# Kernel optimization log

Measured on AMD Instinct MI355X. Metric: run time of the kernel, lower is better.

## Reference

```python
import jax, jax.numpy as jnp
import numpy as np
from jax import lax

BATCH = 4096
HID = 512
T = 20


def setup_inputs() -> dict:
    key = jax.random.key(0)
    ks = jax.random.split(key, 12)
    B2 = BATCH * 2
    inp = {
        "x": jax.random.normal(ks[0], (BATCH, 2, T, 2), jnp.float32),
        "x_agents": jax.random.normal(ks[1], (BATCH, 2), jnp.float32),  # unused by forward
        "h0": jax.random.normal(ks[2], (B2, HID), jnp.float32),
        "c0": jax.random.normal(ks[3], (B2, HID), jnp.float32),
        # LSTMCell params (PyTorch layout: gates stacked as [i, f, g, o])
        "W_ih": jax.random.normal(ks[4], (4 * HID, 2), jnp.float32) * 0.05,
        "W_hh": jax.random.normal(ks[5], (4 * HID, HID), jnp.float32) * 0.05,
        "b_ih": jax.random.normal(ks[6], (4 * HID,), jnp.float32) * 0.05,
        "b_hh": jax.random.normal(ks[7], (4 * HID,), jnp.float32) * 0.05,
        # MLP head
        "fc1_w": jax.random.normal(ks[8], (HID, 2 * T * HID), jnp.float32) * 0.01,
        "fc1_b": jax.random.normal(ks[9], (HID,), jnp.float32) * 0.01,
        "fc2_w": jax.random.normal(ks[10], (1, HID), jnp.float32) * 0.05,
        "fc2_b": jax.random.normal(ks[11], (1,), jnp.float32) * 0.05,
        "training_step": 2,
    }
    return inp


def reference(x, x_agents, h0, c0, W_ih, W_hh, b_ih, b_hh, fc1_w, fc1_b, fc2_w, fc2_b, training_step):
    # training_step == 2 path (default) of the original module.
    batch = x.shape[0]
    H = W_hh.shape[1]
    xs = x.reshape(batch * 2, T, 2).transpose(1, 0, 2)  # [T, B2, 2]

    def step(carry, xt):
        h, c = carry
        gates = xt @ W_ih.T + b_ih + h @ W_hh.T + b_hh  # [B2, 4H]
        i, f, g, o = jnp.split(gates, 4, axis=-1)
        i = jax.nn.sigmoid(i)
        f = jax.nn.sigmoid(f)
        g = jnp.tanh(g)
        o = jax.nn.sigmoid(o)
        c_new = f * c + i * g
        h_new = o * jnp.tanh(c_new)
        return (h_new, c_new), h_new

    _, hs = lax.scan(step, (h0, c0), xs)  # hs: [T, B2, H]
    states = hs.transpose(1, 0, 2).reshape(batch, 2 * T * H)  # [batch, 2*T*H]
    out = jax.nn.relu(states @ fc1_w.T + fc1_b) @ fc2_w.T + fc2_b
    return jax.nn.sigmoid(out)
```

## Files before the change

### kernel.cpp

```cpp
#include <hip/hip_runtime.h>
#include <hip/hip_bf16.h>

#define TSTEPS 20
#define SMEM_BYTES 131072

typedef __bf16 bf16x8 __attribute__((ext_vector_type(8)));
typedef float f32x4 __attribute__((ext_vector_type(4)));
typedef unsigned short u16;

__device__ __forceinline__ u16 f2bf(float f) {
  unsigned u = __builtin_bit_cast(unsigned, f);
  u = (u + 0x7FFFu + ((u >> 16) & 1u)) >> 16;
  return (u16)u;
}
__device__ __forceinline__ float rcp_(float v) { return __builtin_amdgcn_rcpf(v); }
__device__ __forceinline__ float sig_(float v) { return rcp_(1.f + __expf(-v)); }
__device__ __forceinline__ float tanh_(float v) { return 1.f - 2.f * rcp_(1.f + __expf(2.f * v)); }

#define MFMA16(a, b, c) __builtin_amdgcn_mfma_f32_16x16x32_bf16((a), (b), (c), 0, 0, 0)
#define BAR() asm volatile("s_barrier" ::: "memory")
#define WAITV(n) asm volatile("s_waitcnt vmcnt(" #n ")" ::: "memory")
#define WAITLG() asm volatile("s_waitcnt lgkmcnt(0)" ::: "memory")

__device__ __forceinline__ void gload16(const u16* g, u16* lds) {
#if defined(__HIP_DEVICE_COMPILE__)
  __builtin_amdgcn_global_load_lds(
      (const __attribute__((address_space(1))) unsigned*)g,
      (__attribute__((address_space(3))) unsigned*)lds, 16, 0, 0);
#endif
}

__global__ void convert_f32_bf16(const float* __restrict__ s, u16* __restrict__ d, int n) {
  int i = (blockIdx.x * blockDim.x + threadIdx.x) * 4;
  if (i + 3 < n) {
    float4 v = *reinterpret_cast<const float4*>(s + i);
    ushort4 o;
    o.x = f2bf(v.x); o.y = f2bf(v.y); o.z = f2bf(v.z); o.w = f2bf(v.w);
    *reinterpret_cast<ushort4*>(d + i) = o;
  }
}

__global__ void convert_whh_p(const float* __restrict__ w, u16* __restrict__ d) {
  int p = blockIdx.x;
  int k = threadIdx.x;
  int j = p & 15, f = (p >> 4) & 3, wg = (p >> 6) & 3, s = p >> 8;
  int orig = (f << 9) + (s << 6) + (wg << 4) + j;
  d[p * 512 + k] = f2bf(w[orig * 512 + k]);
}

__global__ void bx_prep(const float* __restrict__ Wih, const float* __restrict__ bih,
                        const float* __restrict__ bhh, u16* __restrict__ Bx) {
  int p = blockIdx.x * blockDim.x + threadIdx.x;
  if (p >= 2048) return;
  int j = p & 15, f = (p >> 4) & 3, wg = (p >> 6) & 3, s = p >> 8;
  int o = (f << 9) + (s << 6) + (wg << 4) + j;
  u16* row = Bx + p * 32;
  row[0] = f2bf(Wih[o * 2 + 0]);
  row[1] = f2bf(Wih[o * 2 + 1]);
  row[2] = f2bf(bih[o] + bhh[o]);
#pragma unroll
  for (int k = 3; k < 32; ++k) row[k] = 0;
}

__global__ void init_state(const float* __restrict__ h0, const float* __restrict__ c0,
                           u16* __restrict__ hbf, float* __restrict__ cws,
                           float* __restrict__ acc, int n, int nacc) {
  int i = blockIdx.x * blockDim.x + threadIdx.x;
  if (i < n) { hbf[i] = f2bf(h0[i]); cws[i] = c0[i]; }
  if (i < nacc) acc[i] = 0.f;
}

__global__ __launch_bounds__(512, 1) void step256(
    const u16* __restrict__ Wp,
    const u16* __restrict__ Bxg,
    const float* __restrict__ x,
    const u16* __restrict__ hin,
    u16* __restrict__ hout,
    float* __restrict__ c,
    const u16* __restrict__ fc1w,
    float* __restrict__ facc,
    int t, int doLstm, int doFc1) {
  extern __shared__ char S[];

  const int tid = threadIdx.x;
  const int lane = tid & 63, wid = tid >> 6;
  const int jl = lane & 15, kg = lane >> 4;
  const int bid = blockIdx.x;
  const int s = (bid >> 3) & 7;
  const int nb = (bid & 7) * 4 + (bid >> 6);
  const int n0 = nb * 256;
  const int srow = tid >> 3;
  const int sw = (tid & 7) ^ (srow & 7);

  if (doLstm) {
    const int wm = wid >> 2, wn = wid & 3;
    const int u = s * 64 + wn * 16 + jl;
    const int swz0 = (kg ^ (jl & 7)) * 16;
    const int swz1 = ((4 + kg) ^ (jl & 7)) * 16;
    const int aB0 = wm * 16384 + jl * 128 + swz0;
    const int aB1 = wm * 16384 + jl * 128 + swz1;
    const int bB0 = 32768 + wn * 8192 + jl * 128 + swz0;
    const int bB1 = 32768 + wn * 8192 + jl * 128 + swz1;
    const u16* srcA = hin + (n0 + srow) * 512 + sw * 8;
    const u16* srcB = Wp + (s * 256 + srow) * 512 + sw * 8;

    f32x4 acc[8][4];
#pragma unroll
    for (int mt = 0; mt < 8; ++mt)
#pragma unroll
      for (int f = 0; f < 4; ++f) acc[mt][f] = (f32x4){0.f, 0.f, 0.f, 0.f};

    float2 xv = {0.f, 0.f};
    if (tid < 256) xv = *reinterpret_cast<const float2*>(x + (n0 + tid) * 40 + t * 2);
    {
      const int r0 = tid >> 2, ch = tid & 3;
      gload16(Bxg + (s * 256 + 0 * 128 + r0) * 32 + ch * 8, (u16*)(S + 32768 + 0 * 8192 + wid * 1024));
      gload16(Bxg + (s * 256 + 1 * 128 + r0) * 32 + ch * 8, (u16*)(S + 32768 + 1 * 8192 + wid * 1024));
    }
#pragma unroll
    for (int q = 0; q < 4; ++q) {
      gload16(srcA + q * 32768, (u16*)(S + 65536 + q * 8192 + wid * 1024));
      gload16(srcB + q * 32768, (u16*)(S + 65536 + 32768 + q * 8192 + wid * 1024));
    }
    if (tid < 256) {
      u16 row0[8] = {f2bf(xv.x), f2bf(xv.y), 0x3F80u, 0, 0, 0, 0, 0};
      *reinterpret_cast<uint4*>(S + tid * 64) = *reinterpret_cast<const uint4*>(row0);
      uint4 z = {0u, 0u, 0u, 0u};
      *reinterpret_cast<uint4*>(S + tid * 64 + 16) = z;
      *reinterpret_cast<uint4*>(S + tid * 64 + 32) = z;
      *reinterpret_cast<uint4*>(S + tid * 64 + 48) = z;
    }
    WAITLG();
    WAITV(8);
    BAR();
    {
#pragma unroll
      for (int mt = 0; mt < 8; ++mt) {
        bf16x8 a = *reinterpret_cast<const bf16x8*>(S + (wm * 128 + mt * 16 + jl) * 64 + kg * 16);
#pragma unroll
        for (int f = 0; f < 4; ++f) {
          bf16x8 b = *reinterpret_cast<const bf16x8*>(S + 32768 + (wn * 64 + f * 16 + jl) * 64 + kg * 16);
          acc[mt][f] = MFMA16(a, b, acc[mt][f]);
        }
      }
    }
    BAR();

#define LSTAGE(kt, p)                                                              \
  do {                                                                             \
    _Pragma("unroll") for (int q = 0; q < 4; ++q) {                                \
      gload16(srcA + q * 32768 + (kt) * 64, (u16*)(S + (p) * 65536 + q * 8192 + wid * 1024)); \
      gload16(srcB + q * 32768 + (kt) * 64, (u16*)(S + (p) * 65536 + 32768 + q * 8192 + wid * 1024)); \
    }                                                                              \
  } while (0)
#define LCOMP(p)                                                                   \
  do {                                                                             \
    bf16x8 a0[8], b0[4];                                                           \
    _Pragma("unroll") for (int mt = 0; mt < 8; ++mt)                               \
        a0[mt] = *reinterpret_cast<const bf16x8*>(S + (p) * 65536 + aB0 + mt * 2048); \
    _Pragma("unroll") for (int f = 0; f < 4; ++f)                                  \
        b0[f] = *reinterpret_cast<const bf16x8*>(S + (p) * 65536 + bB0 + f * 2048); \
    _Pragma("unroll") for (int mt = 0; mt < 8; ++mt)                               \
      _Pragma("unroll") for (int f = 0; f < 4; ++f)                                \
        acc[mt][f] = MFMA16(a0[mt], b0[f], acc[mt][f]);                            \
    _Pragma("unroll") for (int mt = 0; mt < 8; ++mt)                               \
        a0[mt] = *reinterpret_cast<const bf16x8*>(S + (p) * 65536 + aB1 + mt * 2048); \
    _Pragma("unroll") for (int f = 0; f < 4; ++f)                                  \
        b0[f] = *reinterpret_cast<const bf16x8*>(S + (p) * 65536 + bB1 + f * 2048); \
    _Pragma("unroll") for (int mt = 0; mt < 8; ++mt)                               \
      _Pragma("unroll") for (int f = 0; f < 4; ++f)                                \
        acc[mt][f] = MFMA16(a0[mt], b0[f], acc[mt][f]);                            \
  } while (0)

#pragma unroll
    for (int kt = 0; kt < 8; ++kt) {
      if (kt < 7) {
        if ((kt + 1) & 1) LSTAGE(kt + 1, 0); else LSTAGE(kt + 1, 1);
        WAITV(8);
      } else {
        WAITV(0);
      }
      BAR();
      if (kt & 1) LCOMP(0); else LCOMP(1);
      BAR();
    }

    float cv[8][4];
#pragma unroll
    for (int mt = 0; mt < 8; ++mt)
#pragma unroll
      for (int r = 0; r < 4; ++r)
        cv[mt][r] = c[(n0 + wm * 128 + mt * 16 + kg * 4 + r) * 512 + u];
#pragma unroll
    for (int mt = 0; mt < 8; ++mt)
#pragma unroll
      for (int r = 0; r < 4; ++r) {
        int n = n0 + wm * 128 + mt * 16 + kg * 4 + r;
        float iv = sig_(acc[mt][0][r]);
        float fv = sig_(acc[mt][1][r]);
        float gv = tanh_(acc[mt][2][r]);
        float ov = sig_(acc[mt][3][r]);
        float cn = fv * cv[mt][r] + iv * gv;
        c[n * 512 + u] = cn;
        hout[n * 512 + u] = f2bf(ov * tanh_(cn));
      }
  }

  if (doFc1) {
    const int Fm0 = nb * 128, Fj0 = s * 64;
    const int Fwm = wid >> 1, Fwn = wid & 1;
    const int tf = t - 1;
    const int swz0 = (kg ^ (jl & 7)) * 16;
    const int swz1 = ((4 + kg) ^ (jl & 7)) * 16;
    const int faB0 = Fwm * 4096 + jl * 128 + swz0;
    const int faB1 = Fwm * 4096 + jl * 128 + swz1;
    const int fbB0 = 16384 + Fwn * 4096 + jl * 128 + swz0;
    const int fbB1 = 16384 + Fwn * 4096 + jl * 128 + swz1;
    const u16* fsrcA = hin + 2 * (Fm0 + srow) * 512 + sw * 8;
    const u16* fsrcB = fc1w + (Fj0 + srow) * 20480 + tf * 512 + sw * 8;

    f32x4 fa[2][2];
#pragma unroll
    for (int a = 0; a < 2; ++a)
#pragma unroll
      for (int b = 0; b < 2; ++b) fa[a][b] = (f32x4){0.f, 0.f, 0.f, 0.f};

#define FSTAGE(kt, p)                                                              \
  do {                                                                             \
    const int an_ = (kt) >> 3, kc_ = ((kt) & 7) * 64;                              \
    gload16(fsrcA + 0 * 65536 + an_ * 512 + kc_, (u16*)(S + (p) * 32768 + 0 * 8192 + wid * 1024)); \
    gload16(fsrcA + 1 * 65536 + an_ * 512 + kc_, (u16*)(S + (p) * 32768 + 1 * 8192 + wid * 1024)); \
    gload16(fsrcB + an_ * 10240 + kc_, (u16*)(S + (p) * 32768 + 16384 + wid * 1024)); \
  } while (0)
#define FCOMP(p)                                                                   \
  do {                                                                             \
    bf16x8 af[2], bf[2];                                                           \
    _Pragma("unroll") for (int mf = 0; mf < 2; ++mf)                               \
        af[mf] = *reinterpret_cast<const bf16x8*>(S + (p) * 32768 + faB0 + mf * 2048); \
    _Pragma("unroll") for (int jf = 0; jf < 2; ++jf)                               \
        bf[jf] = *reinterpret_cast<const bf16x8*>(S + (p) * 32768 + fbB0 + jf * 2048); \
    _Pragma("unroll") for (int mf = 0; mf < 2; ++mf)                               \
      _Pragma("unroll") for (int jf = 0; jf < 2; ++jf)                             \
        fa[mf][jf] = MFMA16(af[mf], bf[jf], fa[mf][jf]);                           \
    _Pragma("unroll") for (int mf = 0; mf < 2; ++mf)                               \
        af[mf] = *reinterpret_cast<const bf16x8*>(S + (p) * 32768 + faB1 + mf * 2048); \
    _Pragma("unroll") for (int jf = 0; jf < 2; ++jf)                               \
        bf[jf] = *reinterpret_cast<const bf16x8*>(S + (p) * 32768 + fbB1 + jf * 2048); \
    _Pragma("unroll") for (int mf = 0; mf < 2; ++mf)                               \
      _Pragma("unroll") for (int jf = 0; jf < 2; ++jf)                             \
        fa[mf][jf] = MFMA16(af[mf], bf[jf], fa[mf][jf]);                           \
  } while (0)

    FSTAGE(0, 0);
#pragma unroll
    for (int kt = 0; kt < 16; ++kt) {
      if (kt < 15) {
        if ((kt + 1) & 1) FSTAGE(kt + 1, 1); else FSTAGE(kt + 1, 0);
        WAITV(3);
      } else {
        WAITV(0);
      }
      BAR();
      if (kt & 1) FCOMP(1); else FCOMP(0);
      BAR();
    }
#pragma unroll
    for (int mf = 0; mf < 2; ++mf)
#pragma unroll
      for (int jf = 0; jf < 2; ++jf) {
        int j = Fj0 + Fwn * 32 + jf * 16 + jl;
#pragma unroll
        for (int r = 0; r < 4; ++r) {
          int m = Fm0 + Fwm * 32 + mf * 16 + kg * 4 + r;
          facc[m * 512 + j] += fa[mf][jf][r];
        }
      }
  }
}

__global__ __launch_bounds__(256) void head_kernel(
    const float* __restrict__ acc, const float* __restrict__ fc1b,
    const float* __restrict__ fc2w, const float* __restrict__ fc2b,
    float* __restrict__ out) {
  int lane = threadIdx.x & 63;
  int row = blockIdx.x * 4 + (threadIdx.x >> 6);
  float sum = 0.f;
#pragma unroll
  for (int j = lane; j < 512; j += 64)
    sum += fmaxf(acc[row * 512 + j] + fc1b[j], 0.f) * fc2w[j];
#pragma unroll
  for (int off = 32; off; off >>= 1) sum += __shfl_down(sum, off);
  if (lane == 0) out[row] = sig_(sum + fc2b[0]);
}

extern "C" void kernel_launch(void* const* d_in, const int* in_sizes, int n_in,
                              void* d_out, int out_size, void* d_ws, size_t ws_size,
                              hipStream_t stream) {
  const float* x = (const float*)d_in[0];
  const float* h0 = (const float*)d_in[2];
  const float* c0 = (const float*)d_in[3];
  const float* Wih = (const float*)d_in[4];
  const float* Whh = (const float*)d_in[5];
  const float* bih = (const float*)d_in[6];
  const float* bhh = (const float*)d_in[7];
  const float* fc1w = (const float*)d_in[8];
  const float* fc1b = (const float*)d_in[9];
  const float* fc2w = (const float*)d_in[10];
  const float* fc2b = (const float*)d_in[11];
  float* out = (float*)d_out;

  char* ws = (char*)d_ws;
  const size_t MB = 1 << 20;
  u16* Wp = (u16*)(ws);
  u16* fc1_bf = (u16*)(ws + 2 * MB);
  u16* hbf0 = (u16*)(ws + 22 * MB);
  u16* hbf1 = (u16*)(ws + 30 * MB);
  float* cws = (float*)(ws + 38 * MB);
  float* facc = (float*)(ws + 54 * MB);
  u16* Bxg = (u16*)(ws + 62 * MB);

  (void)hipFuncSetAttribute(reinterpret_cast<const void*>(step256),
                            hipFuncAttributeMaxDynamicSharedMemorySize, SMEM_BYTES);

  convert_whh_p<<<2048, 512, 0, stream>>>(Whh, Wp);
  bx_prep<<<8, 256, 0, stream>>>(Wih, bih, bhh, Bxg);
  convert_f32_bf16<<<10240, 256, 0, stream>>>(fc1w, fc1_bf, 512 * 20480);
  init_state<<<16384, 256, 0, stream>>>(h0, c0, hbf0, cws, facc, 8192 * 512, 4096 * 512);

  u16* hb[2] = {hbf0, hbf1};
  for (int t = 0; t <= TSTEPS; ++t) {
    step256<<<256, 512, SMEM_BYTES, stream>>>(
        Wp, Bxg, x, hb[t & 1], hb[(t + 1) & 1], cws, fc1_bf, facc,
        t, t < TSTEPS ? 1 : 0, t > 0 ? 1 : 0);
  }
  head_kernel<<<1024, 256, 0, stream>>>(facc, fc1b, fc2w, fc2b, out);
}
```

Baseline: 632.5 us.

## Pre-pack weights into MFMA fragment order and load B operands directly to registers

Weights W_hh and fc1 are repacked once into the exact per-lane MFMA fragment layout, so the step kernel reads B operands straight from global memory into registers instead of staging them through LDS. This halves LDS use (static 64KB instead of 128KB dynamic) and removes the B-side LDS traffic and async copies. The cell state is also stored in a lane-contiguous layout so each thread does vectorized float4 loads and stores of c. The trade-off is more global/L2 load latency on the critical MFMA path, since B fragments are fetched per iteration without LDS double buffering.

```diff
diff --git a/kernel.cpp b/kernel.cpp
--- a/kernel.cpp
+++ b/kernel.cpp
@@ -2,7 +2,6 @@
 #include <hip/hip_bf16.h>
 
 #define TSTEPS 20
-#define SMEM_BYTES 131072
 
 typedef __bf16 bf16x8 __attribute__((ext_vector_type(8)));
 typedef float f32x4 __attribute__((ext_vector_type(4)));
@@ -30,22 +29,37 @@
 #endif
 }
 
-__global__ void convert_f32_bf16(const float* __restrict__ s, u16* __restrict__ d, int n) {
-  int i = (blockIdx.x * blockDim.x + threadIdx.x) * 4;
-  if (i + 3 < n) {
-    float4 v = *reinterpret_cast<const float4*>(s + i);
-    ushort4 o;
-    o.x = f2bf(v.x); o.y = f2bf(v.y); o.z = f2bf(v.z); o.w = f2bf(v.w);
-    *reinterpret_cast<ushort4*>(d + i) = o;
-  }
-}
-
-__global__ void convert_whh_p(const float* __restrict__ w, u16* __restrict__ d) {
-  int p = blockIdx.x;
-  int k = threadIdx.x;
-  int j = p & 15, f = (p >> 4) & 3, wg = (p >> 6) & 3, s = p >> 8;
-  int orig = (f << 9) + (s << 6) + (wg << 4) + j;
-  d[p * 512 + k] = f2bf(w[orig * 512 + k]);
+__global__ void wp2_prep(const float* __restrict__ w, u16* __restrict__ d) {
+  int id = blockIdx.x * blockDim.x + threadIdx.x;
+  int jl = id & 15, t1 = id >> 4;
+  int kg = t1 & 3, t2 = t1 >> 2;
+  int f = t2 & 3, t3 = t2 >> 2;
+  int wn = t3 & 3, t4 = t3 >> 2;
+  int kkg = t4 & 15, s = t4 >> 4;
+  const float* src = w + (f * 512 + s * 64 + wn * 16 + jl) * 512 + kkg * 32 + kg * 8;
+  float4 v0 = *reinterpret_cast<const float4*>(src);
+  float4 v1 = *reinterpret_cast<const float4*>(src + 4);
+  u16* dst = d + id * 8;
+  dst[0] = f2bf(v0.x); dst[1] = f2bf(v0.y); dst[2] = f2bf(v0.z); dst[3] = f2bf(v0.w);
+  dst[4] = f2bf(v1.x); dst[5] = f2bf(v1.y); dst[6] = f2bf(v1.z); dst[7] = f2bf(v1.w);
+}
+
+__global__ void fc1p_prep(const float* __restrict__ w, u16* __restrict__ d) {
+  int id = blockIdx.x * blockDim.x + threadIdx.x;
+  int jl = id & 15, t1 = id >> 4;
+  int kg = t1 & 3, t2 = t1 >> 2;
+  int jf = t2 & 1, t3 = t2 >> 1;
+  int Fwn = t3 & 1, t4 = t3 >> 1;
+  int kk2 = t4 & 31, t5 = t4 >> 5;
+  int tf = t5 % 20, s = t5 / 20;
+  int j = s * 64 + Fwn * 32 + jf * 16 + jl;
+  int k = kk2 * 32 + kg * 8;
+  const float* src = w + j * 20480 + (k >> 9) * 10240 + tf * 512 + (k & 511);
+  float4 v0 = *reinterpret_cast<const float4*>(src);
+  float4 v1 = *reinterpret_cast<const float4*>(src + 4);
+  u16* dst = d + id * 8;
+  dst[0] = f2bf(v0.x); dst[1] = f2bf(v0.y); dst[2] = f2bf(v0.z); dst[3] = f2bf(v0.w);
+  dst[4] = f2bf(v1.x); dst[5] = f2bf(v1.y); dst[6] = f2bf(v1.z); dst[7] = f2bf(v1.w);
 }
 
 __global__ void bx_prep(const float* __restrict__ Wih, const float* __restrict__ bih,
@@ -64,23 +78,32 @@
 
 __global__ void init_state(const float* __restrict__ h0, const float* __restrict__ c0,
                            u16* __restrict__ hbf, float* __restrict__ cws,
-                           float* __restrict__ acc, int n, int nacc) {
+                           float* __restrict__ facc, int nh, int nacc) {
   int i = blockIdx.x * blockDim.x + threadIdx.x;
-  if (i < n) { hbf[i] = f2bf(h0[i]); cws[i] = c0[i]; }
-  if (i < nacc) acc[i] = 0.f;
+  if (i < nh) {
+    hbf[i] = f2bf(h0[i]);
+    int r = i & 3, mt = (i >> 2) & 7, lane = (i >> 5) & 63, wid = (i >> 11) & 7, bid = i >> 14;
+    int s = (bid >> 3) & 7, nb = (bid & 7) * 4 + (bid >> 6);
+    int wm = wid >> 2, wn = wid & 3;
+    int jl = lane & 15, kg = lane >> 4;
+    int n = nb * 256 + wm * 128 + mt * 16 + kg * 4 + r;
+    int u = s * 64 + wn * 16 + jl;
+    cws[i] = c0[n * 512 + u];
+  }
+  if (i < nacc) facc[i] = 0.f;
 }
 
 __global__ __launch_bounds__(512, 1) void step256(
-    const u16* __restrict__ Wp,
+    const u16* __restrict__ Wp2,
     const u16* __restrict__ Bxg,
     const float* __restrict__ x,
     const u16* __restrict__ hin,
     u16* __restrict__ hout,
-    float* __restrict__ c,
-    const u16* __restrict__ fc1w,
+    float* __restrict__ cws,
+    const u16* __restrict__ fc1p,
     float* __restrict__ facc,
     int t, int doLstm, int doFc1) {
-  extern __shared__ char S[];
+  __shared__ char S[65536];
 
   const int tid = threadIdx.x;
   const int lane = tid & 63, wid = tid >> 6;
@@ -91,18 +114,16 @@
   const int n0 = nb * 256;
   const int srow = tid >> 3;
   const int sw = (tid & 7) ^ (srow & 7);
+  const int swz0 = (kg ^ (jl & 7)) * 16;
+  const int swz1 = ((4 + kg) ^ (jl & 7)) * 16;
 
   if (doLstm) {
     const int wm = wid >> 2, wn = wid & 3;
     const int u = s * 64 + wn * 16 + jl;
-    const int swz0 = (kg ^ (jl & 7)) * 16;
-    const int swz1 = ((4 + kg) ^ (jl & 7)) * 16;
     const int aB0 = wm * 16384 + jl * 128 + swz0;
     const int aB1 = wm * 16384 + jl * 128 + swz1;
-    const int bB0 = 32768 + wn * 8192 + jl * 128 + swz0;
-    const int bB1 = 32768 + wn * 8192 + jl * 128 + swz1;
     const u16* srcA = hin + (n0 + srow) * 512 + sw * 8;
-    const u16* srcB = Wp + (s * 256 + srow) * 512 + sw * 8;
+    const u16* bl = Wp2 + s * 131072 + wn * 2048 + kg * 128 + jl * 8;
 
     f32x4 acc[8][4];
 #pragma unroll
@@ -112,112 +133,105 @@
 
     float2 xv = {0.f, 0.f};
     if (tid < 256) xv = *reinterpret_cast<const float2*>(x + (n0 + tid) * 40 + t * 2);
-    {
-      const int r0 = tid >> 2, ch = tid & 3;
-      gload16(Bxg + (s * 256 + 0 * 128 + r0) * 32 + ch * 8, (u16*)(S + 32768 + 0 * 8192 + wid * 1024));
-      gload16(Bxg + (s * 256 + 1 * 128 + r0) * 32 + ch * 8, (u16*)(S + 32768 + 1 * 8192 + wid * 1024));
-    }
-#pragma unroll
-    for (int q = 0; q < 4; ++q) {
-      gload16(srcA + q * 32768, (u16*)(S + 65536 + q * 8192 + wid * 1024));
-      gload16(srcB + q * 32768, (u16*)(S + 65536 + 32768 + q * 8192 + wid * 1024));
-    }
+    gload16(Bxg + (s * 256 + (tid >> 2)) * 32 + (tid & 3) * 8,
+            (u16*)(S + 49152 + wid * 1024));
+    gload16(Bxg + (s * 256 + 128 + (tid >> 2)) * 32 + (tid & 3) * 8,
+            (u16*)(S + 49152 + 8192 + wid * 1024));
+#pragma unroll
+    for (int q = 0; q < 4; ++q)
+      gload16(srcA + q * 32768, (u16*)(S + q * 8192 + wid * 1024));
     if (tid < 256) {
       u16 row0[8] = {f2bf(xv.x), f2bf(xv.y), 0x3F80u, 0, 0, 0, 0, 0};
-      *reinterpret_cast<uint4*>(S + tid * 64) = *reinterpret_cast<const uint4*>(row0);
+      *reinterpret_cast<uint4*>(S + 32768 + tid * 64) = *reinterpret_cast<const uint4*>(row0);
       uint4 z = {0u, 0u, 0u, 0u};
-      *reinterpret_cast<uint4*>(S + tid * 64 + 16) = z;
-      *reinterpret_cast<uint4*>(S + tid * 64 + 32) = z;
-      *reinterpret_cast<uint4*>(S + tid * 64 + 48) = z;
-    }
-    WAITLG();
-    WAITV(8);
+      *reinterpret_cast<uint4*>(S + 32768 + tid * 64 + 16) = z;
+      *reinterpret_cast<uint4*>(S + 32768 + tid * 64 + 32) = z;
+      *reinterpret_cast<uint4*>(S + 32768 + tid * 64 + 48) = z;
+    }
+    WAITV(0); WAITLG();
     BAR();
-    {
-#pragma unroll
-      for (int mt = 0; mt < 8; ++mt) {
-        bf16x8 a = *reinterpret_cast<const bf16x8*>(S + (wm * 128 + mt * 16 + jl) * 64 + kg * 16);
-#pragma unroll
-        for (int f = 0; f < 4; ++f) {
-          bf16x8 b = *reinterpret_cast<const bf16x8*>(S + 32768 + (wn * 64 + f * 16 + jl) * 64 + kg * 16);
-          acc[mt][f] = MFMA16(a, b, acc[mt][f]);
-        }
+#pragma unroll
+    for (int mt = 0; mt < 8; ++mt) {
+      bf16x8 a = *reinterpret_cast<const bf16x8*>(S + 32768 + (wm * 128 + mt * 16 + jl) * 64 + kg * 16);
+#pragma unroll
+      for (int f = 0; f < 4; ++f) {
+        bf16x8 b = *reinterpret_cast<const bf16x8*>(S + 49152 + (wn * 64 + f * 16 + jl) * 64 + kg * 16);
+        acc[mt][f] = MFMA16(a, b, acc[mt][f]);
       }
     }
     BAR();
 
-#define LSTAGE(kt, p)                                                              \
-  do {                                                                             \
-    _Pragma("unroll") for (int q = 0; q < 4; ++q) {                                \
-      gload16(srcA + q * 32768 + (kt) * 64, (u16*)(S + (p) * 65536 + q * 8192 + wid * 1024)); \
-      gload16(srcB + q * 32768 + (kt) * 64, (u16*)(S + (p) * 65536 + 32768 + q * 8192 + wid * 1024)); \
-    }                                                                              \
-  } while (0)
-#define LCOMP(p)                                                                   \
-  do {                                                                             \
-    bf16x8 a0[8], b0[4];                                                           \
-    _Pragma("unroll") for (int mt = 0; mt < 8; ++mt)                               \
-        a0[mt] = *reinterpret_cast<const bf16x8*>(S + (p) * 65536 + aB0 + mt * 2048); \
-    _Pragma("unroll") for (int f = 0; f < 4; ++f)                                  \
-        b0[f] = *reinterpret_cast<const bf16x8*>(S + (p) * 65536 + bB0 + f * 2048); \
-    _Pragma("unroll") for (int mt = 0; mt < 8; ++mt)                               \
-      _Pragma("unroll") for (int f = 0; f < 4; ++f)                                \
-        acc[mt][f] = MFMA16(a0[mt], b0[f], acc[mt][f]);                            \
-    _Pragma("unroll") for (int mt = 0; mt < 8; ++mt)                               \
-        a0[mt] = *reinterpret_cast<const bf16x8*>(S + (p) * 65536 + aB1 + mt * 2048); \
-    _Pragma("unroll") for (int f = 0; f < 4; ++f)                                  \
-        b0[f] = *reinterpret_cast<const bf16x8*>(S + (p) * 65536 + bB1 + f * 2048); \
-    _Pragma("unroll") for (int mt = 0; mt < 8; ++mt)                               \
-      _Pragma("unroll") for (int f = 0; f < 4; ++f)                                \
-        acc[mt][f] = MFMA16(a0[mt], b0[f], acc[mt][f]);                            \
-  } while (0)
-
 #pragma unroll
     for (int kt = 0; kt < 8; ++kt) {
+      bf16x8 bf0[4], bf1[4];
+#pragma unroll
+      for (int f = 0; f < 4; ++f) {
+        bf0[f] = *reinterpret_cast<const bf16x8*>(bl + (kt * 2) * 8192 + f * 512);
+        bf1[f] = *reinterpret_cast<const bf16x8*>(bl + (kt * 2 + 1) * 8192 + f * 512);
+      }
       if (kt < 7) {
-        if ((kt + 1) & 1) LSTAGE(kt + 1, 0); else LSTAGE(kt + 1, 1);
-        WAITV(8);
+        const int p = (kt + 1) & 1;
+        const int kn = (kt + 1) * 64;
+#pragma unroll
+        for (int q = 0; q < 4; ++q)
+          gload16(srcA + q * 32768 + kn, (u16*)(S + p * 32768 + q * 8192 + wid * 1024));
+        WAITV(4);
       } else {
         WAITV(0);
       }
       BAR();
-      if (kt & 1) LCOMP(0); else LCOMP(1);
+      {
+        const int p = kt & 1;
+        bf16x8 a[8];
+#pragma unroll
+        for (int mt = 0; mt < 8; ++mt)
+          a[mt] = *reinterpret_cast<const bf16x8*>(S + p * 32768 + aB0 + mt * 2048);
+#pragma unroll
+        for (int mt = 0; mt < 8; ++mt)
+#pragma unroll
+          for (int f = 0; f < 4; ++f) acc[mt][f] = MFMA16(a[mt], bf0[f], acc[mt][f]);
+#pragma unroll
+        for (int mt = 0; mt < 8; ++mt)
+          a[mt] = *reinterpret_cast<const bf16x8*>(S + p * 32768 + aB1 + mt * 2048);
+#pragma unroll
+        for (int mt = 0; mt < 8; ++mt)
+#pragma unroll
+          for (int f = 0; f < 4; ++f) acc[mt][f] = MFMA16(a[mt], bf1[f], acc[mt][f]);
+      }
       BAR();
     }
 
-    float cv[8][4];
-#pragma unroll
-    for (int mt = 0; mt < 8; ++mt)
-#pragma unroll
-      for (int r = 0; r < 4; ++r)
-        cv[mt][r] = c[(n0 + wm * 128 + mt * 16 + kg * 4 + r) * 512 + u];
-#pragma unroll
-    for (int mt = 0; mt < 8; ++mt)
+    float* cbase = cws + ((bid * 8 + wid) * 64 + lane) * 32;
+#pragma unroll
+    for (int mt = 0; mt < 8; ++mt) {
+      f32x4 cv = *reinterpret_cast<f32x4*>(cbase + mt * 4);
+      f32x4 cn;
+      float hn[4];
 #pragma unroll
       for (int r = 0; r < 4; ++r) {
-        int n = n0 + wm * 128 + mt * 16 + kg * 4 + r;
         float iv = sig_(acc[mt][0][r]);
         float fv = sig_(acc[mt][1][r]);
         float gv = tanh_(acc[mt][2][r]);
         float ov = sig_(acc[mt][3][r]);
-        float cn = fv * cv[mt][r] + iv * gv;
-        c[n * 512 + u] = cn;
-        hout[n * 512 + u] = f2bf(ov * tanh_(cn));
-      }
+        float c2 = fv * cv[r] + iv * gv;
+        cn[r] = c2;
+        hn[r] = ov * tanh_(c2);
+      }
+      *reinterpret_cast<f32x4*>(cbase + mt * 4) = cn;
+#pragma unroll
+      for (int r = 0; r < 4; ++r)
+        hout[(n0 + wm * 128 + mt * 16 + kg * 4 + r) * 512 + u] = f2bf(hn[r]);
+    }
   }
 
   if (doFc1) {
     const int Fm0 = nb * 128, Fj0 = s * 64;
     const int Fwm = wid >> 1, Fwn = wid & 1;
     const int tf = t - 1;
-    const int swz0 = (kg ^ (jl & 7)) * 16;
-    const int swz1 = ((4 + kg) ^ (jl & 7)) * 16;
     const int faB0 = Fwm * 4096 + jl * 128 + swz0;
     const int faB1 = Fwm * 4096 + jl * 128 + swz1;
-    const int fbB0 = 16384 + Fwn * 4096 + jl * 128 + swz0;
-    const int fbB1 = 16384 + Fwn * 4096 + jl * 128 + swz1;
     const u16* fsrcA = hin + 2 * (Fm0 + srow) * 512 + sw * 8;
-    const u16* fsrcB = fc1w + (Fj0 + srow) * 20480 + tf * 512 + sw * 8;
+    const u16* fbl = fc1p + (s * 20 + tf) * 65536 + Fwn * 1024 + kg * 128 + jl * 8;
 
     f32x4 fa[2][2];
 #pragma unroll
@@ -225,43 +239,44 @@
 #pragma unroll
       for (int b = 0; b < 2; ++b) fa[a][b] = (f32x4){0.f, 0.f, 0.f, 0.f};
 
-#define FSTAGE(kt, p)                                                              \
-  do {                                                                             \
-    const int an_ = (kt) >> 3, kc_ = ((kt) & 7) * 64;                              \
-    gload16(fsrcA + 0 * 65536 + an_ * 512 + kc_, (u16*)(S + (p) * 32768 + 0 * 8192 + wid * 1024)); \
-    gload16(fsrcA + 1 * 65536 + an_ * 512 + kc_, (u16*)(S + (p) * 32768 + 1 * 8192 + wid * 1024)); \
-    gload16(fsrcB + an_ * 10240 + kc_, (u16*)(S + (p) * 32768 + 16384 + wid * 1024)); \
-  } while (0)
-#define FCOMP(p)                                                                   \
-  do {                                                                             \
-    bf16x8 af[2], bf[2];                                                           \
-    _Pragma("unroll") for (int mf = 0; mf < 2; ++mf)                               \
-        af[mf] = *reinterpret_cast<const bf16x8*>(S + (p) * 32768 + faB0 + mf * 2048); \
-    _Pragma("unroll") for (int jf = 0; jf < 2; ++jf)                               \
-        bf[jf] = *reinterpret_cast<const bf16x8*>(S + (p) * 32768 + fbB0 + jf * 2048); \
-    _Pragma("unroll") for (int mf = 0; mf < 2; ++mf)                               \
-      _Pragma("unroll") for (int jf = 0; jf < 2; ++jf)                             \
-        fa[mf][jf] = MFMA16(af[mf], bf[jf], fa[mf][jf]);                           \
-    _Pragma("unroll") for (int mf = 0; mf < 2; ++mf)                               \
-        af[mf] = *reinterpret_cast<const bf16x8*>(S + (p) * 32768 + faB1 + mf * 2048); \
-    _Pragma("unroll") for (int jf = 0; jf < 2; ++jf)                               \
-        bf[jf] = *reinterpret_cast<const bf16x8*>(S + (p) * 32768 + fbB1 + jf * 2048); \
-    _Pragma("unroll") for (int mf = 0; mf < 2; ++mf)                               \
-      _Pragma("unroll") for (int jf = 0; jf < 2; ++jf)                             \
-        fa[mf][jf] = MFMA16(af[mf], bf[jf], fa[mf][jf]);                           \
-  } while (0)
-
-    FSTAGE(0, 0);
+    gload16(fsrcA, (u16*)(S + wid * 1024));
+    gload16(fsrcA + 65536, (u16*)(S + 8192 + wid * 1024));
 #pragma unroll
     for (int kt = 0; kt < 16; ++kt) {
+      bf16x8 fb0[2], fb1[2];
+#pragma unroll
+      for (int jf = 0; jf < 2; ++jf) {
+        fb0[jf] = *reinterpret_cast<const bf16x8*>(fbl + (kt * 2) * 2048 + jf * 512);
+        fb1[jf] = *reinterpret_cast<const bf16x8*>(fbl + (kt * 2 + 1) * 2048 + jf * 512);
+      }
       if (kt < 15) {
-        if ((kt + 1) & 1) FSTAGE(kt + 1, 1); else FSTAGE(kt + 1, 0);
-        WAITV(3);
+        const int p = (kt + 1) & 1;
+        const int an = (kt + 1) >> 3, kc = ((kt + 1) & 7) * 64;
+        gload16(fsrcA + an * 512 + kc, (u16*)(S + p * 32768 + wid * 1024));
+        gload16(fsrcA + 65536 + an * 512 + kc, (u16*)(S + p * 32768 + 8192 + wid * 1024));
+        WAITV(2);
       } else {
         WAITV(0);
       }
       BAR();
-      if (kt & 1) FCOMP(1); else FCOMP(0);
+      {
+        const int p = kt & 1;
+        bf16x8 af[2];
+#pragma unroll
+        for (int mf = 0; mf < 2; ++mf)
+          af[mf] = *reinterpret_cast<const bf16x8*>(S + p * 32768 + faB0 + mf * 2048);
+#pragma unroll
+        for (int mf = 0; mf < 2; ++mf)
+#pragma unroll
+          for (int jf = 0; jf < 2; ++jf) fa[mf][jf] = MFMA16(af[mf], fb0[jf], fa[mf][jf]);
+#pragma unroll
+        for (int mf = 0; mf < 2; ++mf)
+          af[mf] = *reinterpret_cast<const bf16x8*>(S + p * 32768 + faB1 + mf * 2048);
+#pragma unroll
+        for (int mf = 0; mf < 2; ++mf)
+#pragma unroll
+          for (int jf = 0; jf < 2; ++jf) fa[mf][jf] = MFMA16(af[mf], fb1[jf], fa[mf][jf]);
+      }
       BAR();
     }
 #pragma unroll
@@ -311,26 +326,23 @@
 
   char* ws = (char*)d_ws;
   const size_t MB = 1 << 20;
-  u16* Wp = (u16*)(ws);
-  u16* fc1_bf = (u16*)(ws + 2 * MB);
+  u16* Wp2 = (u16*)(ws);
+  u16* fc1p = (u16*)(ws + 2 * MB);
   u16* hbf0 = (u16*)(ws + 22 * MB);
   u16* hbf1 = (u16*)(ws + 30 * MB);
   float* cws = (float*)(ws + 38 * MB);
   float* facc = (float*)(ws + 54 * MB);
   u16* Bxg = (u16*)(ws + 62 * MB);
 
-  (void)hipFuncSetAttribute(reinterpret_cast<const void*>(step256),
-                            hipFuncAttributeMaxDynamicSharedMemorySize, SMEM_BYTES);
-
-  convert_whh_p<<<2048, 512, 0, stream>>>(Whh, Wp);
+  wp2_prep<<<512, 256, 0, stream>>>(Whh, Wp2);
+  fc1p_prep<<<2560, 512, 0, stream>>>(fc1w, fc1p);
   bx_prep<<<8, 256, 0, stream>>>(Wih, bih, bhh, Bxg);
-  convert_f32_bf16<<<10240, 256, 0, stream>>>(fc1w, fc1_bf, 512 * 20480);
   init_state<<<16384, 256, 0, stream>>>(h0, c0, hbf0, cws, facc, 8192 * 512, 4096 * 512);
 
   u16* hb[2] = {hbf0, hbf1};
   for (int t = 0; t <= TSTEPS; ++t) {
-    step256<<<256, 512, SMEM_BYTES, stream>>>(
-        Wp, Bxg, x, hb[t & 1], hb[(t + 1) & 1], cws, fc1_bf, facc,
+    step256<<<256, 512, 0, stream>>>(
+        Wp2, Bxg, x, hb[t & 1], hb[(t + 1) & 1], cws, fc1p, facc,
         t, t < TSTEPS ? 1 : 0, t > 0 ? 1 : 0);
   }
   head_kernel<<<1024, 256, 0, stream>>>(facc, fc1b, fc2w, fc2b, out);
```

Result: slower. 892.9 us (+41.2%).
